# Optimization experiments

Measured on AMD Instinct MI355X. Metric: run time of the kernel, lower is better.

The kernel has to match this reference:

```python
import jax, jax.numpy as jnp
import numpy as np

N, E, IN_DIM, HID, OUT = 50000, 800000, 128, 128, 64


def setup_inputs() -> dict:
    key = jax.random.key(0)
    k = jax.random.split(key, 6)
    h = jax.random.normal(k[0], (N, IN_DIM), dtype=jnp.float32)
    edge_index = jax.random.randint(k[1], (2, E), 0, N, dtype=jnp.int64)
    s_in, s_hid = 1.0 / np.sqrt(IN_DIM), 1.0 / np.sqrt(HID)
    W_gcn = jax.random.uniform(k[2], (IN_DIM, HID), jnp.float32, -s_in, s_in)
    b_gcn = jnp.zeros((HID,), jnp.float32)
    W_fc = jax.random.uniform(k[3], (HID, OUT), jnp.float32, -s_hid, s_hid)
    b_fc = jax.random.uniform(k[4], (OUT,), jnp.float32, -s_hid, s_hid)
    return {"h": h, "edge_index": edge_index, "W_gcn": W_gcn,
            "b_gcn": b_gcn, "W_fc": W_fc, "b_fc": b_fc}


def reference(h, edge_index, W_gcn, b_gcn, W_fc, b_fc):
    n = h.shape[0]
    # GCNConv: transform, add self-loops, symmetric normalization, scatter-add
    x = h @ W_gcn                                   # [N, HID]
    loop = jnp.arange(n, dtype=edge_index.dtype)
    row = jnp.concatenate([edge_index[0], loop])    # source nodes
    col = jnp.concatenate([edge_index[1], loop])    # destination nodes
    deg = jax.ops.segment_sum(jnp.ones_like(col, dtype=x.dtype), col,
                              num_segments=n)       # in-degree incl. self-loop
    dinv = jnp.where(deg > 0, jax.lax.rsqrt(deg), 0.0)
    norm = dinv[row] * dinv[col]                    # [E+N]
    msg = x[row] * norm[:, None]                    # gather + scale
    agg = jax.ops.segment_sum(msg, col, num_segments=n) + b_gcn
    # ReLU then projection
    return jax.nn.relu(agg) @ W_fc + b_fc
```

## Files before the change

### kernel.cpp

```cpp
#include <hip/hip_runtime.h>

#define N_NODES 50000
#define N_EDGES 800000
#define NBKT 196
#define BCAP 6144
#define UTS 136
#define GBIN 392

typedef __attribute__((ext_vector_type(4))) float floatx4;
typedef __attribute__((ext_vector_type(8))) _Float16 half8;
typedef __attribute__((ext_vector_type(4))) _Float16 half4;
typedef __attribute__((ext_vector_type(2))) _Float16 half2v;

#define O_PTR   0UL
#define O_GF    200192UL
#define O_DEG   201472UL
#define O_DINV  401664UL
#define O_ESRC  601856UL
#define O_W1    3801856UL
#define O_W2    3834624UL
#define O_STG   3851008UL
#define O_H16   8667904UL

__global__ __launch_bounds__(256) void k_binA(const int* __restrict__ ei,
                                              int* __restrict__ gfill,
                                              unsigned* __restrict__ staging,
                                              int* __restrict__ deg,
                                              const float* __restrict__ Wg,
                                              const float* __restrict__ Wf,
                                              _Float16* __restrict__ W1,
                                              _Float16* __restrict__ W2) {
    int b = blockIdx.x, t = threadIdx.x;
    if (b >= GBIN) {
        int wb = b - GBIN;
        if (wb < 64) {
            int i = wb * 256 + t;
            int n = i >> 7, k = i & 127;
            W1[i] = (_Float16)Wg[k * 128 + n];
        } else {
            int i = (wb - 64) * 256 + t;
            int n = i >> 7, k = i & 127;
            W2[i] = (_Float16)Wf[k * 64 + n];
        }
        return;
    }
    __shared__ int cnt[NBKT];
    __shared__ int gbase[NBKT];
    __shared__ int s_i64;
    if (t < 64) {
        unsigned w = ((const unsigned*)ei)[2 * t + 1];
        unsigned long long m = __ballot(w == 0u);
        if (t == 0) s_i64 = (__popcll(m) >= 60) ? 1 : 0;
    }
    for (int i = t; i < NBKT; i += 256) cnt[i] = 0;
    __syncthreads();
    bool i64 = s_i64 != 0;
    int e0 = b * 2048 + t * 8;
    int sv[8], dvv[8];
    if (i64) {
        const int4* ps = (const int4*)(ei) + (e0 >> 1);
        const int4* pd = (const int4*)(ei + 2 * (size_t)N_EDGES) + (e0 >> 1);
#pragma unroll
        for (int g = 0; g < 4; ++g) {
            if (e0 + 2 * g < N_EDGES) {
                int4 s4 = ps[g], d4 = pd[g];
                sv[2 * g] = s4.x; sv[2 * g + 1] = s4.z;
                dvv[2 * g] = d4.x; dvv[2 * g + 1] = d4.z;
            } else { dvv[2 * g] = -1; dvv[2 * g + 1] = -1; }
        }
    } else {
        const int4* ps = (const int4*)(ei) + (e0 >> 2);
        const int4* pd = (const int4*)(ei + (size_t)N_EDGES) + (e0 >> 2);
#pragma unroll
        for (int g = 0; g < 2; ++g) {
            if (e0 + 4 * g < N_EDGES) {
                int4 s4 = ps[g], d4 = pd[g];
                sv[4 * g] = s4.x; sv[4 * g + 1] = s4.y; sv[4 * g + 2] = s4.z; sv[4 * g + 3] = s4.w;
                dvv[4 * g] = d4.x; dvv[4 * g + 1] = d4.y; dvv[4 * g + 2] = d4.z; dvv[4 * g + 3] = d4.w;
            } else { dvv[4 * g] = -1; dvv[4 * g + 1] = -1; dvv[4 * g + 2] = -1; dvv[4 * g + 3] = -1; }
        }
    }
    unsigned pk[8]; int rk[8]; short bk[8];
#pragma unroll
    for (int j = 0; j < 8; ++j) {
        int d = dvv[j];
        if (d >= 0 && e0 + j < N_EDGES) {
            int bkt = d >> 8;
            bk[j] = (short)bkt;
            pk[j] = (unsigned)sv[j] | ((unsigned)(d & 255) << 16);
            rk[j] = atomicAdd(&cnt[bkt], 1);
            atomicAdd(&deg[d], 1);
        } else bk[j] = -1;
    }
    __syncthreads();
    for (int i = t; i < NBKT; i += 256)
        gbase[i] = atomicAdd(&gfill[i], cnt[i]);
    __syncthreads();
#pragma unroll
    for (int j = 0; j < 8; ++j) {
        if (bk[j] >= 0) {
            int pos = gbase[bk[j]] + rk[j];
            if (pos < BCAP) staging[(size_t)bk[j] * BCAP + pos] = pk[j];
        }
    }
}

__global__ __launch_bounds__(256) void k_binB(const unsigned* __restrict__ staging,
                                              const int* __restrict__ gfill,
                                              const int* __restrict__ deg,
                                              const float* __restrict__ h,
                                              int* __restrict__ ptr,
                                              float* __restrict__ dinv,
                                              _Float16* __restrict__ h16,
                                              int* __restrict__ esrc) {
    int b = blockIdx.x, t = threadIdx.x;
    if (b >= NBKT) {
        __shared__ float sdv[256];
        int nb = (b - NBKT) * 256;
        int nn = min(256, N_NODES - nb);
        if (t < nn) {
            float dv = rsqrtf((float)(deg[nb + t] + 1));
            dinv[nb + t] = dv;
            sdv[t] = dv;
        }
        __syncthreads();
        const floatx4* src = (const floatx4*)(h + (size_t)nb * 128);
        half4* dst = (half4*)(h16 + (size_t)nb * 128);
        int nq = nn * 32;
        for (int i = t; i < nq; i += 256) {
            floatx4 v = src[i];
            float s = sdv[i >> 5];
            half4 o;
            o[0] = (_Float16)(v[0] * s); o[1] = (_Float16)(v[1] * s);
            o[2] = (_Float16)(v[2] * s); o[3] = (_Float16)(v[3] * s);
            dst[i] = o;
        }
        return;
    }
    __shared__ unsigned se[BCAP];
    __shared__ int lcnt[256];
    __shared__ int lscan[256];
    __shared__ int cur[256];
    __shared__ int s_cb;
    int nbase = b * 256;
    int nn = min(256, N_NODES - nbase);
    int cnt = min(gfill[b], BCAP);
    if (t < 64) {
        int acc = 0;
        for (int i = t; i < b; i += 64) acc += min(gfill[i], BCAP);
#pragma unroll
        for (int off = 32; off > 0; off >>= 1) acc += __shfl_down(acc, off);
        if (t == 0) s_cb = acc;
    }
    lcnt[t] = 0;
    __syncthreads();
    int cb = s_cb;
    const unsigned* st = staging + (size_t)b * BCAP;
    for (int i = t; i < cnt; i += 256) {
        unsigned p = st[i];
        se[i] = p;
        atomicAdd(&lcnt[p >> 16], 1);
    }
    __syncthreads();
    int v = lcnt[t];
    lscan[t] = v;
    __syncthreads();
    for (int off = 1; off < 256; off <<= 1) {
        int x = (t >= off) ? lscan[t - off] : 0;
        __syncthreads(); lscan[t] += x; __syncthreads();
    }
    int segstart = cb + (lscan[t] - v);
    if (t < nn) {
        ptr[nbase + t] = segstart;
        cur[t] = segstart;
    }
    __syncthreads();
    for (int i = t; i < cnt; i += 256) {
        unsigned p = se[i];
        int pos = atomicAdd(&cur[p >> 16], 1);
        esrc[pos] = (int)(p & 0xffffu);
    }
}

__global__ __launch_bounds__(256, 8) void k_aggF(const _Float16* __restrict__ h16,
                                                 const int* __restrict__ ptr,
                                                 const int* __restrict__ esrc,
                                                 const float* __restrict__ dinv,
                                                 const _Float16* __restrict__ W1,
                                                 const _Float16* __restrict__ W2,
                                                 const float* __restrict__ bg,
                                                 const float* __restrict__ bfc,
                                                 float* __restrict__ out) {
    __shared__ _Float16 ut[16 * UTS];
    __shared__ _Float16 z[16 * UTS];
    int wave = threadIdx.x >> 6;
    int lane = threadIdx.x & 63;
    int nb = blockIdx.x * 16;
    for (int q = 0; q < 4; ++q) {
        int node = nb + wave * 4 + q;
        int p0 = ptr[node];
        int p1 = (node + 1 < N_NODES) ? ptr[node + 1] : N_EDGES;
        half2v us = *(const half2v*)(h16 + (size_t)node * 128 + lane * 2);
        float a0 = (float)us[0], a1 = (float)us[1];
        for (int base = p0; base < p1; base += 64) {
            int cnt = p1 - base; if (cnt > 64) cnt = 64;
            int idx = 0;
            if (lane < cnt) idx = esrc[base + lane];
            int j = 0;
            for (; j + 8 <= cnt; j += 8) {
                int s0 = __shfl(idx, j),     s1 = __shfl(idx, j + 1);
                int s2 = __shfl(idx, j + 2), s3 = __shfl(idx, j + 3);
                int s4 = __shfl(idx, j + 4), s5 = __shfl(idx, j + 5);
                int s6 = __shfl(idx, j + 6), s7 = __shfl(idx, j + 7);
                half2v u0 = *(const half2v*)(h16 + (size_t)s0 * 128 + lane * 2);
                half2v u1 = *(const half2v*)(h16 + (size_t)s1 * 128 + lane * 2);
                half2v u2 = *(const half2v*)(h16 + (size_t)s2 * 128 + lane * 2);
                half2v u3 = *(const half2v*)(h16 + (size_t)s3 * 128 + lane * 2);
                half2v u4 = *(const half2v*)(h16 + (size_t)s4 * 128 + lane * 2);
                half2v u5 = *(const half2v*)(h16 + (size_t)s5 * 128 + lane * 2);
                half2v u6 = *(const half2v*)(h16 + (size_t)s6 * 128 + lane * 2);
                half2v u7 = *(const half2v*)(h16 + (size_t)s7 * 128 + lane * 2);
                a0 += (float)u0[0] + (float)u1[0] + (float)u2[0] + (float)u3[0]
                    + (float)u4[0] + (float)u5[0] + (float)u6[0] + (float)u7[0];
                a1 += (float)u0[1] + (float)u1[1] + (float)u2[1] + (float)u3[1]
                    + (float)u4[1] + (float)u5[1] + (float)u6[1] + (float)u7[1];
            }
            for (; j + 4 <= cnt; j += 4) {
                int s0 = __shfl(idx, j),     s1 = __shfl(idx, j + 1);
                int s2 = __shfl(idx, j + 2), s3 = __shfl(idx, j + 3);
                half2v u0 = *(const half2v*)(h16 + (size_t)s0 * 128 + lane * 2);
                half2v u1 = *(const half2v*)(h16 + (size_t)s1 * 128 + lane * 2);
                half2v u2 = *(const half2v*)(h16 + (size_t)s2 * 128 + lane * 2);
                half2v u3 = *(const half2v*)(h16 + (size_t)s3 * 128 + lane * 2);
                a0 += (float)u0[0] + (float)u1[0] + (float)u2[0] + (float)u3[0];
                a1 += (float)u0[1] + (float)u1[1] + (float)u2[1] + (float)u3[1];
            }
            for (; j < cnt; ++j) {
                int s = __shfl(idx, j);
                half2v uu = *(const half2v*)(h16 + (size_t)s * 128 + lane * 2);
                a0 += (float)uu[0]; a1 += (float)uu[1];
            }
        }
        float sc = dinv[node];
        int r = wave * 4 + q;
        ut[r * UTS + lane * 2]     = (_Float16)(a0 * sc);
        ut[r * UTS + lane * 2 + 1] = (_Float16)(a1 * sc);
    }
    __syncthreads();
    int quad = lane >> 4, l15 = lane & 15;
    half8 a[4];
#pragma unroll
    for (int kk = 0; kk < 4; ++kk)
        a[kk] = *(const half8*)(ut + l15 * UTS + kk * 32 + quad * 8);
#pragma unroll
    for (int tt = 0; tt < 2; ++tt) {
        floatx4 acc = {0.f, 0.f, 0.f, 0.f};
        int n = (wave * 2 + tt) * 16 + l15;
#pragma unroll
        for (int kk = 0; kk < 4; ++kk) {
            half8 bb = *(const half8*)(W1 + n * 128 + kk * 32 + quad * 8);
            acc = __builtin_amdgcn_mfma_f32_16x16x32_f16(a[kk], bb, acc, 0, 0, 0);
        }
        float bias = bg[n];
#pragma unroll
        for (int i = 0; i < 4; ++i)
            z[(quad * 4 + i) * UTS + n] = (_Float16)fmaxf(acc[i] + bias, 0.f);
    }
    __syncthreads();
    half8 a2[4];
#pragma unroll
    for (int kk = 0; kk < 4; ++kk)
        a2[kk] = *(const half8*)(z + l15 * UTS + kk * 32 + quad * 8);
    {
        floatx4 acc = {0.f, 0.f, 0.f, 0.f};
        int n = wave * 16 + l15;
#pragma unroll
        for (int kk = 0; kk < 4; ++kk) {
            half8 bb = *(const half8*)(W2 + n * 128 + kk * 32 + quad * 8);
            acc = __builtin_amdgcn_mfma_f32_16x16x32_f16(a2[kk], bb, acc, 0, 0, 0);
        }
        float bias = bfc[n];
#pragma unroll
        for (int i = 0; i < 4; ++i)
            out[(size_t)(nb + quad * 4 + i) * 64 + n] = acc[i] + bias;
    }
}

extern "C" void kernel_launch(void* const* d_in, const int* in_sizes, int n_in,
                              void* d_out, int out_size, void* d_ws, size_t ws_size,
                              hipStream_t stream) {
    (void)in_sizes; (void)n_in; (void)out_size; (void)ws_size;
    const float* h  = (const float*)d_in[0];
    const int*   ei = (const int*)d_in[1];
    const float* Wg = (const float*)d_in[2];
    const float* bg = (const float*)d_in[3];
    const float* Wf = (const float*)d_in[4];
    const float* bf = (const float*)d_in[5];
    float* out = (float*)d_out;

    char* ws = (char*)d_ws;
    int*      ptr   = (int*)(ws + O_PTR);
    int*      gfill = (int*)(ws + O_GF);
    int*      deg   = (int*)(ws + O_DEG);
    float*    dinv  = (float*)(ws + O_DINV);
    int*      esrc  = (int*)(ws + O_ESRC);
    _Float16* W1    = (_Float16*)(ws + O_W1);
    _Float16* W2    = (_Float16*)(ws + O_W2);
    unsigned* staging = (unsigned*)(ws + O_STG);
    _Float16* h16   = (_Float16*)(ws + O_H16);

    hipMemsetAsync(ws + O_GF, 0, (size_t)(O_DINV - O_GF), stream);
    k_binA<<<GBIN + 96, 256, 0, stream>>>(ei, gfill, staging, deg, Wg, Wf, W1, W2);
    k_binB<<<NBKT + 196, 256, 0, stream>>>(staging, gfill, deg, h, ptr, dinv, h16, esrc);
    k_aggF<<<N_NODES / 16, 256, 0, stream>>>(h16, ptr, esrc, dinv,
                                             W1, W2, bg, bf, out);
}
```

Measured before the change: 181.6 us.

## Derive degrees from bucket counts, drop global degree atomics, split conversion kernel

Removes the per-edge global atomicAdd on the degree array and instead computes each node's in-degree from the per-node local count already built in the bucket sort kernel, writing dinv there. Each binning block now handles 16 edges per thread instead of 8, which halves the block count. The fp16 scaling of h moves into a separate kernel launched after binB, because it needs dinv. This cuts global atomic traffic and shrinks the memset, at the cost of one extra launch and serialising the h conversion after binning instead of overlapping it.

```diff
diff --git a/kernel.cpp b/kernel.cpp
--- a/kernel.cpp
+++ b/kernel.cpp
@@ -5,7 +5,6 @@
 #define NBKT 196
 #define BCAP 6144
 #define UTS 136
-#define GBIN 392
 
 typedef __attribute__((ext_vector_type(4))) float floatx4;
 typedef __attribute__((ext_vector_type(8))) _Float16 half8;
@@ -14,7 +13,6 @@
 
 #define O_PTR   0UL
 #define O_GF    200192UL
-#define O_DEG   201472UL
 #define O_DINV  401664UL
 #define O_ESRC  601856UL
 #define O_W1    3801856UL
@@ -25,14 +23,13 @@
 __global__ __launch_bounds__(256) void k_binA(const int* __restrict__ ei,
                                               int* __restrict__ gfill,
                                               unsigned* __restrict__ staging,
-                                              int* __restrict__ deg,
                                               const float* __restrict__ Wg,
                                               const float* __restrict__ Wf,
                                               _Float16* __restrict__ W1,
                                               _Float16* __restrict__ W2) {
     int b = blockIdx.x, t = threadIdx.x;
-    if (b >= GBIN) {
-        int wb = b - GBIN;
+    if (b >= NBKT) {
+        int wb = b - NBKT;
         if (wb < 64) {
             int i = wb * 256 + t;
             int n = i >> 7, k = i & 127;
@@ -55,13 +52,13 @@
     for (int i = t; i < NBKT; i += 256) cnt[i] = 0;
     __syncthreads();
     bool i64 = s_i64 != 0;
-    int e0 = b * 2048 + t * 8;
-    int sv[8], dvv[8];
+    int e0 = b * 4096 + t * 16;
+    int sv[16], dvv[16];
     if (i64) {
         const int4* ps = (const int4*)(ei) + (e0 >> 1);
         const int4* pd = (const int4*)(ei + 2 * (size_t)N_EDGES) + (e0 >> 1);
 #pragma unroll
-        for (int g = 0; g < 4; ++g) {
+        for (int g = 0; g < 8; ++g) {
             if (e0 + 2 * g < N_EDGES) {
                 int4 s4 = ps[g], d4 = pd[g];
                 sv[2 * g] = s4.x; sv[2 * g + 1] = s4.z;
@@ -72,7 +69,7 @@
         const int4* ps = (const int4*)(ei) + (e0 >> 2);
         const int4* pd = (const int4*)(ei + (size_t)N_EDGES) + (e0 >> 2);
 #pragma unroll
-        for (int g = 0; g < 2; ++g) {
+        for (int g = 0; g < 4; ++g) {
             if (e0 + 4 * g < N_EDGES) {
                 int4 s4 = ps[g], d4 = pd[g];
                 sv[4 * g] = s4.x; sv[4 * g + 1] = s4.y; sv[4 * g + 2] = s4.z; sv[4 * g + 3] = s4.w;
@@ -80,16 +77,15 @@
             } else { dvv[4 * g] = -1; dvv[4 * g + 1] = -1; dvv[4 * g + 2] = -1; dvv[4 * g + 3] = -1; }
         }
     }
-    unsigned pk[8]; int rk[8]; short bk[8];
-#pragma unroll
-    for (int j = 0; j < 8; ++j) {
+    unsigned pk[16]; int rk[16]; short bk[16];
+#pragma unroll
+    for (int j = 0; j < 16; ++j) {
         int d = dvv[j];
         if (d >= 0 && e0 + j < N_EDGES) {
             int bkt = d >> 8;
             bk[j] = (short)bkt;
             pk[j] = (unsigned)sv[j] | ((unsigned)(d & 255) << 16);
             rk[j] = atomicAdd(&cnt[bkt], 1);
-            atomicAdd(&deg[d], 1);
         } else bk[j] = -1;
     }
     __syncthreads();
@@ -97,7 +93,7 @@
         gbase[i] = atomicAdd(&gfill[i], cnt[i]);
     __syncthreads();
 #pragma unroll
-    for (int j = 0; j < 8; ++j) {
+    for (int j = 0; j < 16; ++j) {
         if (bk[j] >= 0) {
             int pos = gbase[bk[j]] + rk[j];
             if (pos < BCAP) staging[(size_t)bk[j] * BCAP + pos] = pk[j];
@@ -107,41 +103,15 @@
 
 __global__ __launch_bounds__(256) void k_binB(const unsigned* __restrict__ staging,
                                               const int* __restrict__ gfill,
-                                              const int* __restrict__ deg,
-                                              const float* __restrict__ h,
                                               int* __restrict__ ptr,
                                               float* __restrict__ dinv,
-                                              _Float16* __restrict__ h16,
                                               int* __restrict__ esrc) {
-    int b = blockIdx.x, t = threadIdx.x;
-    if (b >= NBKT) {
-        __shared__ float sdv[256];
-        int nb = (b - NBKT) * 256;
-        int nn = min(256, N_NODES - nb);
-        if (t < nn) {
-            float dv = rsqrtf((float)(deg[nb + t] + 1));
-            dinv[nb + t] = dv;
-            sdv[t] = dv;
-        }
-        __syncthreads();
-        const floatx4* src = (const floatx4*)(h + (size_t)nb * 128);
-        half4* dst = (half4*)(h16 + (size_t)nb * 128);
-        int nq = nn * 32;
-        for (int i = t; i < nq; i += 256) {
-            floatx4 v = src[i];
-            float s = sdv[i >> 5];
-            half4 o;
-            o[0] = (_Float16)(v[0] * s); o[1] = (_Float16)(v[1] * s);
-            o[2] = (_Float16)(v[2] * s); o[3] = (_Float16)(v[3] * s);
-            dst[i] = o;
-        }
-        return;
-    }
     __shared__ unsigned se[BCAP];
     __shared__ int lcnt[256];
     __shared__ int lscan[256];
     __shared__ int cur[256];
     __shared__ int s_cb;
+    int b = blockIdx.x, t = threadIdx.x;
     int nbase = b * 256;
     int nn = min(256, N_NODES - nbase);
     int cnt = min(gfill[b], BCAP);
@@ -171,7 +141,9 @@
     }
     int segstart = cb + (lscan[t] - v);
     if (t < nn) {
-        ptr[nbase + t] = segstart;
+        int node = nbase + t;
+        ptr[node] = segstart;
+        dinv[node] = rsqrtf((float)(v + 1));
         cur[t] = segstart;
     }
     __syncthreads();
@@ -179,6 +151,29 @@
         unsigned p = se[i];
         int pos = atomicAdd(&cur[p >> 16], 1);
         esrc[pos] = (int)(p & 0xffffu);
+    }
+}
+
+__global__ __launch_bounds__(256) void k_conv(const float* __restrict__ h,
+                                              const float* __restrict__ dinv,
+                                              _Float16* __restrict__ h16) {
+    __shared__ float sdv[128];
+    int b = blockIdx.x, t = threadIdx.x;
+    int nb = b * 128;
+    int nn = min(128, N_NODES - nb);
+    if (nn <= 0) return;
+    if (t < nn) sdv[t] = dinv[nb + t];
+    __syncthreads();
+    const floatx4* src = (const floatx4*)(h + (size_t)nb * 128);
+    half4* dst = (half4*)(h16 + (size_t)nb * 128);
+    int nq = nn * 32;
+    for (int i = t; i < nq; i += 256) {
+        floatx4 v = src[i];
+        float s = sdv[i >> 5];
+        half4 o;
+        o[0] = (_Float16)(v[0] * s); o[1] = (_Float16)(v[1] * s);
+        o[2] = (_Float16)(v[2] * s); o[3] = (_Float16)(v[3] * s);
+        dst[i] = o;
     }
 }
 
@@ -301,7 +296,6 @@
     char* ws = (char*)d_ws;
     int*      ptr   = (int*)(ws + O_PTR);
     int*      gfill = (int*)(ws + O_GF);
-    int*      deg   = (int*)(ws + O_DEG);
     float*    dinv  = (float*)(ws + O_DINV);
     int*      esrc  = (int*)(ws + O_ESRC);
     _Float16* W1    = (_Float16*)(ws + O_W1);
@@ -309,9 +303,10 @@
     unsigned* staging = (unsigned*)(ws + O_STG);
     _Float16* h16   = (_Float16*)(ws + O_H16);
 
-    hipMemsetAsync(ws + O_GF, 0, (size_t)(O_DINV - O_GF), stream);
-    k_binA<<<GBIN + 96, 256, 0, stream>>>(ei, gfill, staging, deg, Wg, Wf, W1, W2);
-    k_binB<<<NBKT + 196, 256, 0, stream>>>(staging, gfill, deg, h, ptr, dinv, h16, esrc);
+    hipMemsetAsync(gfill, 0, NBKT * sizeof(int), stream);
+    k_binA<<<NBKT + 96, 256, 0, stream>>>(ei, gfill, staging, Wg, Wf, W1, W2);
+    k_binB<<<NBKT, 256, 0, stream>>>(staging, gfill, ptr, dinv, esrc);
+    k_conv<<<(N_NODES + 127) / 128, 256, 0, stream>>>(h, dinv, h16);
     k_aggF<<<N_NODES / 16, 256, 0, stream>>>(h16, ptr, esrc, dinv,
                                              W1, W2, bg, bf, out);
 }
```

Result: faster. 161.7 us (-10.9%).

## Fuse binning and CSR build into one cooperative kernel with grid syncs

Applied to the files above, without the earlier changes.

Merges the memset, binning and CSR-construction kernels into a single cooperative kernel that uses grid-wide syncs between phases. Global atomics on the bucket fill counters and on the per-node degrees are replaced by a per-block count matrix with a deterministic prefix scan. Degrees now come from the per-bucket local histogram, which removes the separate deg array and its memset. The cost is four grid barriers across 392 blocks, which must all be co-resident, and less overlap between phases.

```diff
diff --git a/kernel.cpp b/kernel.cpp
--- a/kernel.cpp
+++ b/kernel.cpp
@@ -1,11 +1,14 @@
 #include <hip/hip_runtime.h>
+#include <hip/hip_cooperative_groups.h>
+
+namespace cg = cooperative_groups;
 
 #define N_NODES 50000
 #define N_EDGES 800000
 #define NBKT 196
+#define NBIN 392
 #define BCAP 6144
 #define UTS 136
-#define GBIN 392
 
 typedef __attribute__((ext_vector_type(4))) float floatx4;
 typedef __attribute__((ext_vector_type(8))) _Float16 half8;
@@ -14,39 +17,44 @@
 
 #define O_PTR   0UL
 #define O_GF    200192UL
-#define O_DEG   201472UL
-#define O_DINV  401664UL
-#define O_ESRC  601856UL
-#define O_W1    3801856UL
-#define O_W2    3834624UL
-#define O_STG   3851008UL
-#define O_H16   8667904UL
-
-__global__ __launch_bounds__(256) void k_binA(const int* __restrict__ ei,
-                                              int* __restrict__ gfill,
-                                              unsigned* __restrict__ staging,
-                                              int* __restrict__ deg,
-                                              const float* __restrict__ Wg,
-                                              const float* __restrict__ Wf,
-                                              _Float16* __restrict__ W1,
-                                              _Float16* __restrict__ W2) {
+#define O_C     201216UL
+#define O_B     508672UL
+#define O_DINV  816128UL
+#define O_ESRC  1016320UL
+#define O_W1    4216320UL
+#define O_W2    4249088UL
+#define O_STG   4265472UL
+#define O_H16   9082368UL
+
+__global__ __launch_bounds__(256) void k_pre(const int* __restrict__ ei,
+                                             const float* __restrict__ h,
+                                             const float* __restrict__ Wg,
+                                             const float* __restrict__ Wf,
+                                             int* __restrict__ gfill,
+                                             int* __restrict__ C,
+                                             int* __restrict__ B,
+                                             int* __restrict__ ptr,
+                                             float* __restrict__ dinv,
+                                             int* __restrict__ esrc,
+                                             _Float16* __restrict__ W1,
+                                             _Float16* __restrict__ W2,
+                                             unsigned* __restrict__ staging,
+                                             _Float16* __restrict__ h16) {
+    cg::grid_group grid = cg::this_grid();
     int b = blockIdx.x, t = threadIdx.x;
-    if (b >= GBIN) {
-        int wb = b - GBIN;
-        if (wb < 64) {
-            int i = wb * 256 + t;
-            int n = i >> 7, k = i & 127;
-            W1[i] = (_Float16)Wg[k * 128 + n];
-        } else {
-            int i = (wb - 64) * 256 + t;
-            int n = i >> 7, k = i & 127;
-            W2[i] = (_Float16)Wf[k * 64 + n];
-        }
-        return;
-    }
+
+    for (int i = b * 256 + t; i < 16384; i += NBIN * 256) {
+        int n = i >> 7, k = i & 127;
+        W1[i] = (_Float16)Wg[k * 128 + n];
+    }
+    for (int i = b * 256 + t; i < 8192; i += NBIN * 256) {
+        int n = i >> 7, k = i & 127;
+        W2[i] = (_Float16)Wf[k * 64 + n];
+    }
+
     __shared__ int cnt[NBKT];
-    __shared__ int gbase[NBKT];
     __shared__ int s_i64;
+    __shared__ int s_cb;
     if (t < 64) {
         unsigned w = ((const unsigned*)ei)[2 * t + 1];
         unsigned long long m = __ballot(w == 0u);
@@ -89,12 +97,32 @@
             bk[j] = (short)bkt;
             pk[j] = (unsigned)sv[j] | ((unsigned)(d & 255) << 16);
             rk[j] = atomicAdd(&cnt[bkt], 1);
-            atomicAdd(&deg[d], 1);
         } else bk[j] = -1;
     }
     __syncthreads();
     for (int i = t; i < NBKT; i += 256)
-        gbase[i] = atomicAdd(&gfill[i], cnt[i]);
+        C[i * NBIN + b] = cnt[i];
+    grid.sync();
+
+    __shared__ int sA[NBIN], sB[NBIN];
+    if (b < NBKT) {
+        for (int i = t; i < NBIN; i += 256) sA[i] = C[b * NBIN + i];
+        __syncthreads();
+        int* src = sA; int* dst = sB;
+        for (int off = 1; off < NBIN; off <<= 1) {
+            for (int i = t; i < NBIN; i += 256)
+                dst[i] = src[i] + ((i >= off) ? src[i - off] : 0);
+            __syncthreads();
+            int* tmp = src; src = dst; dst = tmp;
+        }
+        for (int i = t; i < NBIN; i += 256)
+            B[b * NBIN + i] = src[i] - C[b * NBIN + i];
+        if (t == 0) gfill[b] = src[NBIN - 1];
+    }
+    grid.sync();
+
+    __shared__ int gbase[NBKT];
+    for (int i = t; i < NBKT; i += 256) gbase[i] = B[i * NBIN + b];
     __syncthreads();
 #pragma unroll
     for (int j = 0; j < 8; ++j) {
@@ -103,82 +131,77 @@
             if (pos < BCAP) staging[(size_t)bk[j] * BCAP + pos] = pk[j];
         }
     }
-}
-
-__global__ __launch_bounds__(256) void k_binB(const unsigned* __restrict__ staging,
-                                              const int* __restrict__ gfill,
-                                              const int* __restrict__ deg,
-                                              const float* __restrict__ h,
-                                              int* __restrict__ ptr,
-                                              float* __restrict__ dinv,
-                                              _Float16* __restrict__ h16,
-                                              int* __restrict__ esrc) {
-    int b = blockIdx.x, t = threadIdx.x;
-    if (b >= NBKT) {
-        __shared__ float sdv[256];
-        int nb = (b - NBKT) * 256;
-        int nn = min(256, N_NODES - nb);
-        if (t < nn) {
-            float dv = rsqrtf((float)(deg[nb + t] + 1));
-            dinv[nb + t] = dv;
-            sdv[t] = dv;
-        }
-        __syncthreads();
-        const floatx4* src = (const floatx4*)(h + (size_t)nb * 128);
-        half4* dst = (half4*)(h16 + (size_t)nb * 128);
-        int nq = nn * 32;
-        for (int i = t; i < nq; i += 256) {
-            floatx4 v = src[i];
-            float s = sdv[i >> 5];
-            half4 o;
-            o[0] = (_Float16)(v[0] * s); o[1] = (_Float16)(v[1] * s);
-            o[2] = (_Float16)(v[2] * s); o[3] = (_Float16)(v[3] * s);
-            dst[i] = o;
-        }
-        return;
-    }
+    grid.sync();
+
     __shared__ unsigned se[BCAP];
     __shared__ int lcnt[256];
     __shared__ int lscan[256];
     __shared__ int cur[256];
-    __shared__ int s_cb;
-    int nbase = b * 256;
-    int nn = min(256, N_NODES - nbase);
-    int cnt = min(gfill[b], BCAP);
-    if (t < 64) {
-        int acc = 0;
-        for (int i = t; i < b; i += 64) acc += min(gfill[i], BCAP);
-#pragma unroll
-        for (int off = 32; off > 0; off >>= 1) acc += __shfl_down(acc, off);
-        if (t == 0) s_cb = acc;
-    }
-    lcnt[t] = 0;
-    __syncthreads();
-    int cb = s_cb;
-    const unsigned* st = staging + (size_t)b * BCAP;
-    for (int i = t; i < cnt; i += 256) {
-        unsigned p = st[i];
-        se[i] = p;
-        atomicAdd(&lcnt[p >> 16], 1);
-    }
-    __syncthreads();
-    int v = lcnt[t];
-    lscan[t] = v;
-    __syncthreads();
-    for (int off = 1; off < 256; off <<= 1) {
-        int x = (t >= off) ? lscan[t - off] : 0;
-        __syncthreads(); lscan[t] += x; __syncthreads();
-    }
-    int segstart = cb + (lscan[t] - v);
-    if (t < nn) {
-        ptr[nbase + t] = segstart;
-        cur[t] = segstart;
-    }
-    __syncthreads();
-    for (int i = t; i < cnt; i += 256) {
-        unsigned p = se[i];
-        int pos = atomicAdd(&cur[p >> 16], 1);
-        esrc[pos] = (int)(p & 0xffffu);
+    int csr_cnt = 0;
+    if (b < NBKT) {
+        int nbase = b * 256;
+        int nn = min(256, N_NODES - nbase);
+        csr_cnt = min(gfill[b], BCAP);
+        if (t < 64) {
+            int acc = 0;
+            for (int i = t; i < b; i += 64) acc += min(gfill[i], BCAP);
+#pragma unroll
+            for (int off = 32; off > 0; off >>= 1) acc += __shfl_down(acc, off);
+            if (t == 0) s_cb = acc;
+        }
+        lcnt[t] = 0;
+        __syncthreads();
+        int cb = s_cb;
+        const unsigned* st = staging + (size_t)b * BCAP;
+        for (int i = t; i < csr_cnt; i += 256) {
+            unsigned p = st[i];
+            se[i] = p;
+            atomicAdd(&lcnt[p >> 16], 1);
+        }
+        __syncthreads();
+        int v = lcnt[t];
+        lscan[t] = v;
+        __syncthreads();
+        for (int off = 1; off < 256; off <<= 1) {
+            int x = (t >= off) ? lscan[t - off] : 0;
+            __syncthreads(); lscan[t] += x; __syncthreads();
+        }
+        int segstart = cb + (lscan[t] - v);
+        if (t < nn) {
+            int node = nbase + t;
+            ptr[node] = segstart;
+            dinv[node] = rsqrtf((float)(v + 1));
+            cur[t] = segstart;
+        }
+        __syncthreads();
+    }
+    grid.sync();
+
+    if (b < NBKT) {
+        for (int i = t; i < csr_cnt; i += 256) {
+            unsigned p = se[i];
+            int pos = atomicAdd(&cur[p >> 16], 1);
+            esrc[pos] = (int)(p & 0xffffu);
+        }
+    } else {
+        __shared__ float sdv[256];
+        int nb = (b - NBKT) * 256;
+        int nn = min(256, N_NODES - nb);
+        if (nn > 0) {
+            if (t < nn) sdv[t] = dinv[nb + t];
+            __syncthreads();
+            const floatx4* src = (const floatx4*)(h + (size_t)nb * 128);
+            half4* dst = (half4*)(h16 + (size_t)nb * 128);
+            int nq = nn * 32;
+            for (int i = t; i < nq; i += 256) {
+                floatx4 v = src[i];
+                float s = sdv[i >> 5];
+                half4 o;
+                o[0] = (_Float16)(v[0] * s); o[1] = (_Float16)(v[1] * s);
+                o[2] = (_Float16)(v[2] * s); o[3] = (_Float16)(v[3] * s);
+                dst[i] = o;
+            }
+        }
     }
 }
 
@@ -301,7 +324,8 @@
     char* ws = (char*)d_ws;
     int*      ptr   = (int*)(ws + O_PTR);
     int*      gfill = (int*)(ws + O_GF);
-    int*      deg   = (int*)(ws + O_DEG);
+    int*      C     = (int*)(ws + O_C);
+    int*      B     = (int*)(ws + O_B);
     float*    dinv  = (float*)(ws + O_DINV);
     int*      esrc  = (int*)(ws + O_ESRC);
     _Float16* W1    = (_Float16*)(ws + O_W1);
@@ -309,9 +333,12 @@
     unsigned* staging = (unsigned*)(ws + O_STG);
     _Float16* h16   = (_Float16*)(ws + O_H16);
 
-    hipMemsetAsync(ws + O_GF, 0, (size_t)(O_DINV - O_GF), stream);
-    k_binA<<<GBIN + 96, 256, 0, stream>>>(ei, gfill, staging, deg, Wg, Wf, W1, W2);
-    k_binB<<<NBKT + 196, 256, 0, stream>>>(staging, gfill, deg, h, ptr, dinv, h16, esrc);
+    void* args[] = { (void*)&ei, (void*)&h, (void*)&Wg, (void*)&Wf,
+                     (void*)&gfill, (void*)&C, (void*)&B, (void*)&ptr,
+                     (void*)&dinv, (void*)&esrc, (void*)&W1, (void*)&W2,
+                     (void*)&staging, (void*)&h16 };
+    hipLaunchCooperativeKernel((void*)k_pre, dim3(NBIN), dim3(256),
+                               args, 0, stream);
     k_aggF<<<N_NODES / 16, 256, 0, stream>>>(h16, ptr, esrc, dinv,
                                              W1, W2, bg, bf, out);
 }
```

Result: slower. 341.2 us (+87.9%).
